# Kernel optimization log

Measured on AMD Instinct MI355X. Metric: run time of the kernel, lower is better.

## Reference

```python
import jax, jax.numpy as jnp
import numpy as np

COEF_MEMORY = 0.2


def setup_inputs() -> dict:
    key = jax.random.key(0)
    k0, k1, k2, k3 = jax.random.split(key, 4)
    bs, T, h, w, ck, cv, M = 8, 8, 32, 32, 256, 3, 512
    return {
        "k": jax.random.normal(k0, (bs, T, h, w, ck), dtype=jnp.float32),
        "v": jax.random.normal(k1, (bs, T, h, w, cv), dtype=jnp.float32),
        "m_k": jax.random.normal(k2, (bs, T, M, ck), dtype=jnp.float32),
        "m_v": jax.random.normal(k3, (bs, T, M, cv), dtype=jnp.float32),
    }


def reference(k, v, m_k, m_v):
    # k: [bs, T, h, w, ck]; v: [bs, T, h, w, cv]
    # m_k: [bs, T, M, ck]; m_v: [bs, T, M, cv]
    bs, T, h, w, ck = k.shape
    cv = v.shape[-1]
    hw = h * w
    k_flat = k.reshape(bs, T, hw, ck)
    v_flat = v.reshape(bs, T, hw, cv)

    # queries: frame i+1 tokens; keys: frame i tokens (unscaled inner product)
    q = k_flat[:, 1:]            # [bs, T-1, hw, ck]
    ref = k_flat[:, :-1]         # [bs, T-1, hw, ck]
    sim_k = jax.nn.softmax(jnp.einsum('btqc,btkc->btqk', q, ref), axis=-1)  # [bs,T-1,hw,hw]
    recon_k = jnp.einsum('btqk,btkv->btqv', sim_k, v_flat[:, :-1])          # [bs,T-1,hw,cv]

    # frame-to-memory attention against memory at step i
    sim_m = jax.nn.softmax(jnp.einsum('btqc,btmc->btqm', q, m_k[:, :-1]), axis=-1)  # [bs,T-1,hw,M]
    recon_m = jnp.einsum('btqm,btmv->btqv', sim_m, m_v[:, :-1])                     # [bs,T-1,hw,cv]

    output_v = (1.0 - COEF_MEMORY) * recon_k + COEF_MEMORY * recon_m  # [bs,T-1,hw,cv]
    ground_truth = v[:, 1:]                                           # [bs,T-1,h,w,cv]
    return output_v, ground_truth
```

## Files before the change

### kernel.cpp

```cpp
#include <hip/hip_runtime.h>
#include <stdint.h>

typedef _Float16 f16x8 __attribute__((ext_vector_type(8)));
typedef __bf16 bf16x8 __attribute__((ext_vector_type(8)));
typedef float f32x4 __attribute__((ext_vector_type(4)));

#define MFMA_F16(a,b,c) __builtin_amdgcn_mfma_f32_16x16x32_f16(a,b,c,0,0,0)
#define MFMA_BF16(a,b,c) __builtin_amdgcn_mfma_f32_16x16x32_bf16(a,b,c,0,0,0)
#define ALPHA 1.2011224087864498f

__device__ __forceinline__ uint32_t f2u(float x){ union{float f;uint32_t u;} c; c.f=x; return c.u; }
__device__ __forceinline__ float u2f(uint32_t u){ union{float f;uint32_t u;} c; c.u=u; return c.f; }

union HU8 { uint32_t u[4]; _Float16 h[8]; f16x8 v; };

__device__ __forceinline__ void split_pair(float x0, float x1, uint32_t& hp, uint32_t& lp){
  uint32_t u0=f2u(x0), u1=f2u(x1);
  uint32_t h0=u0&0xFFFF0000u, h1=u1&0xFFFF0000u;
  hp = (u0>>16) | h1;
  float l0 = x0 - u2f(h0), l1 = x1 - u2f(h1);
  lp = (f2u(l0)>>16) | (f2u(l1)&0xFFFF0000u);
}

__device__ __forceinline__ void glds16(const void* g, void* l){
  __builtin_amdgcn_global_load_lds(
      (const __attribute__((address_space(1))) uint32_t*)(uintptr_t)g,
      (__attribute__((address_space(3))) uint32_t*)(uint32_t)(uintptr_t)l,
      16, 0, 0);
}

__global__ void kast_cvt3(const float* __restrict__ K_, const float* __restrict__ MK_,
                          uint4* __restrict__ khi, uint4* __restrict__ mkhi){
  int i = blockIdx.x*256 + threadIdx.x;
  const float* src; uint4* hi; int j;
  if (i < 2097152){ src = K_;  hi = khi;  j = i; }
  else            { src = MK_; hi = mkhi; j = i - 2097152; }
  const float4* in4 = (const float4*)src;
  float4 a = in4[(size_t)j*2], c = in4[(size_t)j*2+1];
  HU8 h;
  h.h[0]=(_Float16)(a.x*ALPHA); h.h[1]=(_Float16)(a.y*ALPHA);
  h.h[2]=(_Float16)(a.z*ALPHA); h.h[3]=(_Float16)(a.w*ALPHA);
  h.h[4]=(_Float16)(c.x*ALPHA); h.h[5]=(_Float16)(c.y*ALPHA);
  h.h[6]=(_Float16)(c.z*ALPHA); h.h[7]=(_Float16)(c.w*ALPHA);
  hi[j] = make_uint4(h.u[0],h.u[1],h.u[2],h.u[3]);
}

__launch_bounds__(256, 2)
__global__ void kast_attn9(const ushort* __restrict__ khi, const ushort* __restrict__ mkhi,
                           const float* __restrict__ V_, const float* __restrict__ MV_,
                           float* __restrict__ part) {
  __shared__ uint8_t KB[2][16384];
  __shared__ float vlds[1536];

  const int bid = blockIdx.x;
  const int xcd = bid & 7;
  const int idx = bid >> 3;
  const int grp = idx / 24;
  const int sub = idx - grp*24;
  const int s   = xcd + 8*grp;
  const int qb  = sub & 7;
  const int ks  = sub >> 3;
  const int b = s / 7, t = s % 7;

  const uint8_t* kh8; const float* vbase;
  if (ks < 2){
    size_t row0 = (size_t)((b*8 + t)*1024 + ks*512);
    kh8 = (const uint8_t*)khi + row0*512;
    vbase = V_ + row0*3;
  } else {
    size_t row0 = (size_t)((b*8 + t)*512);
    kh8 = (const uint8_t*)mkhi + row0*512;
    vbase = MV_ + row0*3;
  }

  const int tid = threadIdx.x;
  const int w = tid >> 6, l = tid & 63;
  const int lj = l & 15, lq = l >> 4;
  const int qrow0 = qb*128 + w*32;

  for (int i = tid; i < 1536; i += 256) vlds[i] = vbase[i];

  const uint8_t* q8 = (const uint8_t*)khi + (size_t)((b*8 + t + 1)*1024)*512;
  f16x8 qh[2][8];
#pragma unroll
  for (int rt=0; rt<2; rt++){
    const uint8_t* qr = q8 + (size_t)(qrow0 + rt*16 + lj)*512 + lq*16;
#pragma unroll
    for (int kc=0; kc<8; kc++)
      qh[rt][kc] = *(const f16x8*)(qr + kc*64);
  }

  float m[2][4], ssum[2][4], o[2][4][3];
#pragma unroll
  for (int rt=0;rt<2;rt++)
#pragma unroll
    for (int r=0;r<4;r++){
      m[rt][r]=-1e30f; ssum[rt][r]=0.f;
      o[rt][r][0]=0.f; o[rt][r][1]=0.f; o[rt][r][2]=0.f;
    }

  const int sg = l & 31;
  const int rsub = l >> 5;

  #define ISSUE_TILE(NT, P) do{                                              \
    _Pragma("unroll")                                                        \
    for (int i_=0;i_<4;i_++){                                                \
      int lrow_ = (w<<3) + (i_<<1) + rsub;                                   \
      size_t soff_ = (size_t)((NT)*32 + lrow_)*512 + (size_t)((sg ^ (lrow_&7))<<4); \
      uint32_t dbase_ = ((w<<3) + (i_<<1))*512;                              \
      glds16(kh8 + soff_, &KB[(P)][dbase_]);                                 \
    } }while(0)

  ISSUE_TILE(0, 0);
  __syncthreads();

  for (int nt=0; nt<16; nt++){
    const int cur = nt & 1;
    if (nt < 15){
      ISSUE_TILE(nt+1, cur^1);
      asm volatile("s_waitcnt vmcnt(4)" ::: "memory");
    } else {
      asm volatile("s_waitcnt vmcnt(0)" ::: "memory");
    }
    asm volatile("s_barrier" ::: "memory");

    f32x4 acc[2][2];
#pragma unroll
    for (int rt=0;rt<2;rt++){ acc[rt][0]=(f32x4){0,0,0,0}; acc[rt][1]=(f32x4){0,0,0,0}; }

    const int sx = (l&7)<<4;
#pragma unroll
    for (int ct=0;ct<2;ct++){
      const uint8_t* rb = &KB[cur][(ct*16 + lj)*512];
#pragma unroll
      for (int kc=0;kc<8;kc++){
        int bo = (kc*64 + (lq<<4)) ^ sx;
        f16x8 bh = *(const f16x8*)(rb + bo);
        acc[0][ct] = MFMA_F16(qh[0][kc], bh, acc[0][ct]);
        acc[1][ct] = MFMA_F16(qh[1][kc], bh, acc[1][ct]);
      }
    }

    float vv[2][3];
#pragma unroll
    for (int ct=0;ct<2;ct++){
      int c = (nt*32 + ct*16 + lj)*3;
      vv[ct][0]=vlds[c]; vv[ct][1]=vlds[c+1]; vv[ct][2]=vlds[c+2];
    }
#pragma unroll
    for (int rt=0;rt<2;rt++)
#pragma unroll
      for (int r=0;r<4;r++){
        float s0=acc[rt][0][r], s1=acc[rt][1][r];
        float mo = m[rt][r];
        float mn = fmaxf(mo, fmaxf(s0,s1));
        float sc = exp2f(mo - mn);
        float p0 = exp2f(s0 - mn), p1 = exp2f(s1 - mn);
        ssum[rt][r] = ssum[rt][r]*sc + (p0 + p1);
        o[rt][r][0] = o[rt][r][0]*sc + p0*vv[0][0] + p1*vv[1][0];
        o[rt][r][1] = o[rt][r][1]*sc + p0*vv[0][1] + p1*vv[1][1];
        o[rt][r][2] = o[rt][r][2]*sc + p0*vv[0][2] + p1*vv[1][2];
        m[rt][r]=mn;
      }

    asm volatile("s_barrier" ::: "memory");
  }

#pragma unroll
  for (int rt=0;rt<2;rt++)
#pragma unroll
    for (int r=0;r<4;r++){
      float mm = m[rt][r];
      mm = fmaxf(mm, __shfl_xor(mm,1));
      mm = fmaxf(mm, __shfl_xor(mm,2));
      mm = fmaxf(mm, __shfl_xor(mm,4));
      mm = fmaxf(mm, __shfl_xor(mm,8));
      float f = exp2f(m[rt][r]-mm);
      float sl = ssum[rt][r]*f;
      float o0=o[rt][r][0]*f, o1=o[rt][r][1]*f, o2=o[rt][r][2]*f;
      sl += __shfl_xor(sl,1); sl += __shfl_xor(sl,2); sl += __shfl_xor(sl,4); sl += __shfl_xor(sl,8);
      o0 += __shfl_xor(o0,1); o0 += __shfl_xor(o0,2); o0 += __shfl_xor(o0,4); o0 += __shfl_xor(o0,8);
      o1 += __shfl_xor(o1,1); o1 += __shfl_xor(o1,2); o1 += __shfl_xor(o1,4); o1 += __shfl_xor(o1,8);
      o2 += __shfl_xor(o2,1); o2 += __shfl_xor(o2,2); o2 += __shfl_xor(o2,4); o2 += __shfl_xor(o2,8);
      if (lj == 0){
        int prow = qrow0 + rt*16 + lq*4 + r;
        float* pp = part + ((size_t)(s*3 + ks)*1024 + prow)*5;
        pp[0]=mm; pp[1]=sl; pp[2]=o0; pp[3]=o1; pp[4]=o2;
      }
    }
  #undef ISSUE_TILE
}

__global__ void kast_merge(const float* __restrict__ part, float* __restrict__ OUT_){
  int r = blockIdx.x*256 + threadIdx.x;
  if (r >= 56*1024) return;
  int s = r >> 10, row = r & 1023;
  const float* pa = part + ((size_t)(s*3+0)*1024 + row)*5;
  const float* pb = part + ((size_t)(s*3+1)*1024 + row)*5;
  const float* pm = part + ((size_t)(s*3+2)*1024 + row)*5;
  float ma=pa[0], sa=pa[1], mb=pb[0], sb=pb[1];
  float M = fmaxf(ma,mb);
  float ea = exp2f(ma-M), eb = exp2f(mb-M);
  float w1 = 0.8f / (sa*ea + sb*eb);
  float w2 = 0.2f / pm[1];
  float* op = OUT_ + (size_t)(s*1024 + row)*3;
  op[0] = (pa[2]*ea + pb[2]*eb)*w1 + pm[2]*w2;
  op[1] = (pa[3]*ea + pb[3]*eb)*w1 + pm[3]*w2;
  op[2] = (pa[4]*ea + pb[4]*eb)*w1 + pm[4]*w2;
}

__launch_bounds__(256, 2)
__global__ void kast_attn_fb(const float* __restrict__ K_, const float* __restrict__ V_,
                             const float* __restrict__ MK_, const float* __restrict__ MV_,
                             float* __restrict__ OUT_) {
  __shared__ char KhB[64*512];
  __shared__ char KlB[64*512];
  __shared__ float vlds[192];

  const int bid = blockIdx.x;
  const int s  = ((bid>>6)<<3) | (bid & 7);
  const int qb = (bid>>3) & 7;
  const int b = s / 7, t = s % 7;
  const float* qptr = K_ + (size_t)((b*8 + t + 1) * 1024) * 256;
  const float* k1   = K_ + (size_t)((b*8 + t) * 1024) * 256;
  const float* v1   = V_ + (size_t)((b*8 + t) * 1024) * 3;
  const float* k2   = MK_ + (size_t)((b*8 + t) * 512) * 256;
  const float* v2   = MV_ + (size_t)((b*8 + t) * 512) * 3;
  float* outp = OUT_ + (size_t)((b*7 + t) * 1024) * 3;

  const int tid = threadIdx.x;
  const int w = tid >> 6, l = tid & 63;
  const int lj = l & 15, lq = l >> 4;
  const int qrow0 = qb*128 + w*32;

  bf16x8 qh[2][8], ql[2][8];
#pragma unroll
  for (int rt=0; rt<2; rt++){
    const float* qr = qptr + (size_t)(qrow0 + rt*16 + lj)*256 + lq*8;
#pragma unroll
    for (int kc=0; kc<8; kc++){
      float4 a = *(const float4*)(qr + kc*32);
      float4 c = *(const float4*)(qr + kc*32 + 4);
      union { uint32_t d[4]; bf16x8 v; } hh, ll;
      split_pair(a.x, a.y, hh.d[0], ll.d[0]);
      split_pair(a.z, a.w, hh.d[1], ll.d[1]);
      split_pair(c.x, c.y, hh.d[2], ll.d[2]);
      split_pair(c.z, c.w, hh.d[3], ll.d[3]);
      qh[rt][kc]=hh.v; ql[rt][kc]=ll.v;
    }
  }

  for (int ph=0; ph<2; ph++){
    const float* ks = ph ? k2 : k1;
    const float* vs = ph ? v2 : v1;
    const int ntiles = ph ? 8 : 16;
    float m[2][4], ssum[2][4], o[2][4][3];
#pragma unroll
    for (int rt=0;rt<2;rt++)
#pragma unroll
      for (int r=0;r<4;r++){
        m[rt][r]=-1e30f; ssum[rt][r]=0.f;
        o[rt][r][0]=0.f; o[rt][r][1]=0.f; o[rt][r][2]=0.f;
      }

    for (int nt=0; nt<ntiles; nt++){
      __syncthreads();
      const float* kt = ks + (size_t)nt*64*256;
#pragma unroll 4
      for (int i=0;i<16;i++){
        int f4i = tid + i*256;
        int row = f4i >> 6;
        int col4 = f4i & 63;
        float4 x = *(const float4*)(kt + row*256 + col4*4);
        uint32_t hp0,lp0,hp1,lp1;
        split_pair(x.x,x.y,hp0,lp0);
        split_pair(x.z,x.w,hp1,lp1);
        int boff = row*512 + ((col4*8) ^ ((row&7)<<4));
        *(uint2*)(KhB + boff) = make_uint2(hp0,hp1);
        *(uint2*)(KlB + boff) = make_uint2(lp0,lp1);
      }
      if (tid < 192) vlds[tid] = vs[nt*192 + tid];
      __syncthreads();

      f32x4 acc[2][4];
#pragma unroll
      for (int rt=0;rt<2;rt++)
#pragma unroll
        for (int ct=0;ct<4;ct++)
          acc[rt][ct] = (f32x4){0.f,0.f,0.f,0.f};

      const int sx = (l&7)<<4;
#pragma unroll
      for (int ct=0;ct<4;ct++){
        const char* rbh = KhB + (ct*16 + lj)*512;
        const char* rbl = KlB + (ct*16 + lj)*512;
#pragma unroll
        for (int kc=0;kc<8;kc++){
          int bo = (kc*64 + (lq<<4)) ^ sx;
          bf16x8 bh = *(const bf16x8*)(rbh + bo);
          bf16x8 bl = *(const bf16x8*)(rbl + bo);
          acc[0][ct] = MFMA_BF16(qh[0][kc], bh, acc[0][ct]);
          acc[1][ct] = MFMA_BF16(qh[1][kc], bh, acc[1][ct]);
          acc[0][ct] = MFMA_BF16(qh[0][kc], bl, acc[0][ct]);
          acc[1][ct] = MFMA_BF16(qh[1][kc], bl, acc[1][ct]);
          acc[0][ct] = MFMA_BF16(ql[0][kc], bh, acc[0][ct]);
          acc[1][ct] = MFMA_BF16(ql[1][kc], bh, acc[1][ct]);
        }
      }

      float vv[4][3];
#pragma unroll
      for (int ct=0;ct<4;ct++){
        int c = (ct*16 + lj)*3;
        vv[ct][0]=vlds[c]; vv[ct][1]=vlds[c+1]; vv[ct][2]=vlds[c+2];
      }
#pragma unroll
      for (int rt=0;rt<2;rt++)
#pragma unroll
        for (int r=0;r<4;r++){
          float s0=acc[rt][0][r], s1=acc[rt][1][r], s2=acc[rt][2][r], s3=acc[rt][3][r];
          float tmax = fmaxf(fmaxf(s0,s1),fmaxf(s2,s3));
          float mo = m[rt][r];
          float mn = fmaxf(mo, tmax);
          float sc = __expf(mo - mn);
          float p0=__expf(s0-mn), p1=__expf(s1-mn), p2=__expf(s2-mn), p3=__expf(s3-mn);
          ssum[rt][r] = ssum[rt][r]*sc + ((p0+p1)+(p2+p3));
          o[rt][r][0] = o[rt][r][0]*sc + (p0*vv[0][0]+p1*vv[1][0]) + (p2*vv[2][0]+p3*vv[3][0]);
          o[rt][r][1] = o[rt][r][1]*sc + (p0*vv[0][1]+p1*vv[1][1]) + (p2*vv[2][1]+p3*vv[3][1]);
          o[rt][r][2] = o[rt][r][2]*sc + (p0*vv[0][2]+p1*vv[1][2]) + (p2*vv[2][2]+p3*vv[3][2]);
          m[rt][r]=mn;
        }
    }

    const float coef = ph ? 0.2f : 0.8f;
#pragma unroll
    for (int rt=0;rt<2;rt++)
#pragma unroll
      for (int r=0;r<4;r++){
        float mm = m[rt][r];
        mm = fmaxf(mm, __shfl_xor(mm,1));
        mm = fmaxf(mm, __shfl_xor(mm,2));
        mm = fmaxf(mm, __shfl_xor(mm,4));
        mm = fmaxf(mm, __shfl_xor(mm,8));
        float f = __expf(m[rt][r]-mm);
        float sl = ssum[rt][r]*f;
        float o0=o[rt][r][0]*f, o1=o[rt][r][1]*f, o2=o[rt][r][2]*f;
        sl += __shfl_xor(sl,1); sl += __shfl_xor(sl,2); sl += __shfl_xor(sl,4); sl += __shfl_xor(sl,8);
        o0 += __shfl_xor(o0,1); o0 += __shfl_xor(o0,2); o0 += __shfl_xor(o0,4); o0 += __shfl_xor(o0,8);
        o1 += __shfl_xor(o1,1); o1 += __shfl_xor(o1,2); o1 += __shfl_xor(o1,4); o1 += __shfl_xor(o1,8);
        o2 += __shfl_xor(o2,1); o2 += __shfl_xor(o2,2); o2 += __shfl_xor(o2,4); o2 += __shfl_xor(o2,8);
        if (lj == 0){
          int row = qrow0 + rt*16 + lq*4 + r;
          float* op = outp + (size_t)row*3;
          float invs = coef / sl;
          if (ph==0){ op[0]=o0*invs; op[1]=o1*invs; op[2]=o2*invs; }
          else      { op[0]+=o0*invs; op[1]+=o1*invs; op[2]+=o2*invs; }
        }
      }
  }
}

__global__ void kast_gt(const float* __restrict__ V_, float* __restrict__ OUT_){
  int s = blockIdx.x; int b = s/7, t = s%7;
  const float4* src = (const float4*)(V_ + (size_t)(b*8+t+1)*3072);
  float4* dst = (float4*)(OUT_ + 172032 + (size_t)s*3072);
  for (int i=threadIdx.x; i<768; i+=256) dst[i] = src[i];
}

extern "C" void kernel_launch(void* const* d_in, const int* in_sizes, int n_in,
                              void* d_out, int out_size, void* d_ws, size_t ws_size,
                              hipStream_t stream) {
  (void)in_sizes; (void)n_in; (void)out_size;
  const float* K_  = (const float*)d_in[0];
  const float* V_  = (const float*)d_in[1];
  const float* MK_ = (const float*)d_in[2];
  const float* MV_ = (const float*)d_in[3];
  float* out = (float*)d_out;

  const size_t NEED = 53772288;
  if (ws_size >= NEED){
    uint8_t* w8 = (uint8_t*)d_ws;
    ushort* khi  = (ushort*)(w8);
    ushort* mkhi = (ushort*)(w8 + 33554432);
    float*  part = (float*)(w8 + 50331648);
    hipLaunchKernelGGL(kast_cvt3, dim3(12288), dim3(256), 0, stream, K_, MK_,
                       (uint4*)khi, (uint4*)mkhi);
    hipLaunchKernelGGL(kast_attn9, dim3(1344), dim3(256), 0, stream, khi, mkhi, V_, MV_, part);
    hipLaunchKernelGGL(kast_merge, dim3(224),  dim3(256), 0, stream, part, out);
  } else {
    hipLaunchKernelGGL(kast_attn_fb, dim3(448), dim3(256), 0, stream, K_, V_, MK_, MV_, out);
  }
  hipLaunchKernelGGL(kast_gt, dim3(56), dim3(256), 0, stream, V_, out);
}
```

Measured before the change: 124.7 us.

## Load key tiles directly into registers and skip softmax rescale lazily

Drops the LDS double-buffered global_load_lds staging of key tiles and the per-iteration barriers. Each wave now loads its B operands straight from global memory into registers, software-pipelined between two 16-column halves, and raises wave priority around MFMA bursts. It also adds a lazy online-softmax rescale that only updates the running max when a new score exceeds it by more than 24 (log2 units). The cost is that all four waves redundantly fetch the same key rows from global/L2 instead of sharing them through LDS, and the register load rises.

```diff
diff --git a/kernel.cpp b/kernel.cpp
--- a/kernel.cpp
+++ b/kernel.cpp
@@ -20,13 +20,6 @@
   hp = (u0>>16) | h1;
   float l0 = x0 - u2f(h0), l1 = x1 - u2f(h1);
   lp = (f2u(l0)>>16) | (f2u(l1)&0xFFFF0000u);
-}
-
-__device__ __forceinline__ void glds16(const void* g, void* l){
-  __builtin_amdgcn_global_load_lds(
-      (const __attribute__((address_space(1))) uint32_t*)(uintptr_t)g,
-      (__attribute__((address_space(3))) uint32_t*)(uint32_t)(uintptr_t)l,
-      16, 0, 0);
 }
 
 __global__ void kast_cvt3(const float* __restrict__ K_, const float* __restrict__ MK_,
@@ -46,10 +39,9 @@
 }
 
 __launch_bounds__(256, 2)
-__global__ void kast_attn9(const ushort* __restrict__ khi, const ushort* __restrict__ mkhi,
-                           const float* __restrict__ V_, const float* __restrict__ MV_,
-                           float* __restrict__ part) {
-  __shared__ uint8_t KB[2][16384];
+__global__ void kast_attn10(const ushort* __restrict__ khi, const ushort* __restrict__ mkhi,
+                            const float* __restrict__ V_, const float* __restrict__ MV_,
+                            float* __restrict__ part) {
   __shared__ float vlds[1536];
 
   const int bid = blockIdx.x;
@@ -89,6 +81,7 @@
     for (int kc=0; kc<8; kc++)
       qh[rt][kc] = *(const f16x8*)(qr + kc*64);
   }
+  __syncthreads();
 
   float m[2][4], ssum[2][4], o[2][4][3];
 #pragma unroll
@@ -99,47 +92,42 @@
       o[rt][r][0]=0.f; o[rt][r][1]=0.f; o[rt][r][2]=0.f;
     }
 
-  const int sg = l & 31;
-  const int rsub = l >> 5;
-
-  #define ISSUE_TILE(NT, P) do{                                              \
-    _Pragma("unroll")                                                        \
-    for (int i_=0;i_<4;i_++){                                                \
-      int lrow_ = (w<<3) + (i_<<1) + rsub;                                   \
-      size_t soff_ = (size_t)((NT)*32 + lrow_)*512 + (size_t)((sg ^ (lrow_&7))<<4); \
-      uint32_t dbase_ = ((w<<3) + (i_<<1))*512;                              \
-      glds16(kh8 + soff_, &KB[(P)][dbase_]);                                 \
-    } }while(0)
-
-  ISSUE_TILE(0, 0);
-  __syncthreads();
+  const uint8_t* kp0 = kh8 + (size_t)(lj*512 + lq*16);
+  const uint8_t* kp1 = kp0 + 16*512;
+
+  f16x8 ka[8], kb[8];
+#pragma unroll
+  for (int kc=0;kc<8;kc++) ka[kc] = *(const f16x8*)(kp0 + kc*64);
 
   for (int nt=0; nt<16; nt++){
-    const int cur = nt & 1;
+#pragma unroll
+    for (int kc=0;kc<8;kc++) kb[kc] = *(const f16x8*)(kp1 + kc*64);
+
+    f32x4 acc[2][2];
+#pragma unroll
+    for (int rt=0;rt<2;rt++){ acc[rt][0]=(f32x4){0,0,0,0}; acc[rt][1]=(f32x4){0,0,0,0}; }
+
+    __builtin_amdgcn_s_setprio(1);
+#pragma unroll
+    for (int kc=0;kc<8;kc++){
+      acc[0][0] = MFMA_F16(qh[0][kc], ka[kc], acc[0][0]);
+      acc[1][0] = MFMA_F16(qh[1][kc], ka[kc], acc[1][0]);
+    }
+    __builtin_amdgcn_s_setprio(0);
+
+    kp0 += 16384; kp1 += 16384;
     if (nt < 15){
-      ISSUE_TILE(nt+1, cur^1);
-      asm volatile("s_waitcnt vmcnt(4)" ::: "memory");
-    } else {
-      asm volatile("s_waitcnt vmcnt(0)" ::: "memory");
-    }
-    asm volatile("s_barrier" ::: "memory");
-
-    f32x4 acc[2][2];
-#pragma unroll
-    for (int rt=0;rt<2;rt++){ acc[rt][0]=(f32x4){0,0,0,0}; acc[rt][1]=(f32x4){0,0,0,0}; }
-
-    const int sx = (l&7)<<4;
-#pragma unroll
-    for (int ct=0;ct<2;ct++){
-      const uint8_t* rb = &KB[cur][(ct*16 + lj)*512];
-#pragma unroll
-      for (int kc=0;kc<8;kc++){
-        int bo = (kc*64 + (lq<<4)) ^ sx;
-        f16x8 bh = *(const f16x8*)(rb + bo);
-        acc[0][ct] = MFMA_F16(qh[0][kc], bh, acc[0][ct]);
-        acc[1][ct] = MFMA_F16(qh[1][kc], bh, acc[1][ct]);
-      }
-    }
+#pragma unroll
+      for (int kc=0;kc<8;kc++) ka[kc] = *(const f16x8*)(kp0 + kc*64);
+    }
+
+    __builtin_amdgcn_s_setprio(1);
+#pragma unroll
+    for (int kc=0;kc<8;kc++){
+      acc[0][1] = MFMA_F16(qh[0][kc], kb[kc], acc[0][1]);
+      acc[1][1] = MFMA_F16(qh[1][kc], kb[kc], acc[1][1]);
+    }
+    __builtin_amdgcn_s_setprio(0);
 
     float vv[2][3];
 #pragma unroll
@@ -147,23 +135,38 @@
       int c = (nt*32 + ct*16 + lj)*3;
       vv[ct][0]=vlds[c]; vv[ct][1]=vlds[c+1]; vv[ct][2]=vlds[c+2];
     }
+    float pm[2][4];
+    float need = -1e30f;
 #pragma unroll
     for (int rt=0;rt<2;rt++)
 #pragma unroll
       for (int r=0;r<4;r++){
-        float s0=acc[rt][0][r], s1=acc[rt][1][r];
-        float mo = m[rt][r];
-        float mn = fmaxf(mo, fmaxf(s0,s1));
-        float sc = exp2f(mo - mn);
-        float p0 = exp2f(s0 - mn), p1 = exp2f(s1 - mn);
-        ssum[rt][r] = ssum[rt][r]*sc + (p0 + p1);
-        o[rt][r][0] = o[rt][r][0]*sc + p0*vv[0][0] + p1*vv[1][0];
-        o[rt][r][1] = o[rt][r][1]*sc + p0*vv[0][1] + p1*vv[1][1];
-        o[rt][r][2] = o[rt][r][2]*sc + p0*vv[0][2] + p1*vv[1][2];
-        m[rt][r]=mn;
-      }
-
-    asm volatile("s_barrier" ::: "memory");
+        pm[rt][r] = fmaxf(acc[rt][0][r], acc[rt][1][r]);
+        need = fmaxf(need, pm[rt][r] - m[rt][r]);
+      }
+    if (need > 24.f){
+#pragma unroll
+      for (int rt=0;rt<2;rt++)
+#pragma unroll
+        for (int r=0;r<4;r++){
+          float mn = fmaxf(m[rt][r], pm[rt][r]);
+          float sc = exp2f(m[rt][r] - mn);
+          ssum[rt][r] *= sc;
+          o[rt][r][0] *= sc; o[rt][r][1] *= sc; o[rt][r][2] *= sc;
+          m[rt][r] = mn;
+        }
+    }
+#pragma unroll
+    for (int rt=0;rt<2;rt++)
+#pragma unroll
+      for (int r=0;r<4;r++){
+        float p0 = exp2f(acc[rt][0][r] - m[rt][r]);
+        float p1 = exp2f(acc[rt][1][r] - m[rt][r]);
+        ssum[rt][r] += p0 + p1;
+        o[rt][r][0] += p0*vv[0][0] + p1*vv[1][0];
+        o[rt][r][1] += p0*vv[0][1] + p1*vv[1][1];
+        o[rt][r][2] += p0*vv[0][2] + p1*vv[1][2];
+      }
   }
 
 #pragma unroll
@@ -188,7 +191,6 @@
         pp[0]=mm; pp[1]=sl; pp[2]=o0; pp[3]=o1; pp[4]=o2;
       }
     }
-  #undef ISSUE_TILE
 }
 
 __global__ void kast_merge(const float* __restrict__ part, float* __restrict__ OUT_){
@@ -385,7 +387,7 @@
     float*  part = (float*)(w8 + 50331648);
     hipLaunchKernelGGL(kast_cvt3, dim3(12288), dim3(256), 0, stream, K_, MK_,
                        (uint4*)khi, (uint4*)mkhi);
-    hipLaunchKernelGGL(kast_attn9, dim3(1344), dim3(256), 0, stream, khi, mkhi, V_, MV_, part);
+    hipLaunchKernelGGL(kast_attn10, dim3(1344), dim3(256), 0, stream, khi, mkhi, V_, MV_, part);
     hipLaunchKernelGGL(kast_merge, dim3(224),  dim3(256), 0, stream, part, out);
   } else {
     hipLaunchKernelGGL(kast_attn_fb, dim3(448), dim3(256), 0, stream, K_, V_, MK_, MV_, out);
```

Measured after the change: 214.9 us. +72.4%, slower.

## Double block size to 512 threads and add lazy softmax rescaling

Applied to the files above, without the earlier changes.

Each attention block now uses 8 waves covering 256 query rows instead of 4 waves covering 128, so each K tile staged in LDS is reused by twice as many queries and each thread issues half as many async loads. The online softmax now skips the running-max rescale unless some row's new max exceeds the stored max by more than a threshold of 24 in log2 units. This saves exp2 calls and multiplies per tile. The trade-offs are half as many blocks, one block per CU under the new launch bounds, and wider barriers across 8 waves. The rescale threshold relies on fp32 headroom to avoid overflow.

```diff
diff --git a/kernel.cpp b/kernel.cpp
--- a/kernel.cpp
+++ b/kernel.cpp
@@ -45,21 +45,21 @@
   hi[j] = make_uint4(h.u[0],h.u[1],h.u[2],h.u[3]);
 }
 
-__launch_bounds__(256, 2)
-__global__ void kast_attn9(const ushort* __restrict__ khi, const ushort* __restrict__ mkhi,
-                           const float* __restrict__ V_, const float* __restrict__ MV_,
-                           float* __restrict__ part) {
+__launch_bounds__(512, 1)
+__global__ void kast_attn11(const ushort* __restrict__ khi, const ushort* __restrict__ mkhi,
+                            const float* __restrict__ V_, const float* __restrict__ MV_,
+                            float* __restrict__ part) {
   __shared__ uint8_t KB[2][16384];
   __shared__ float vlds[1536];
 
   const int bid = blockIdx.x;
   const int xcd = bid & 7;
   const int idx = bid >> 3;
-  const int grp = idx / 24;
-  const int sub = idx - grp*24;
+  const int grp = idx / 12;
+  const int sub = idx - grp*12;
   const int s   = xcd + 8*grp;
-  const int qb  = sub & 7;
-  const int ks  = sub >> 3;
+  const int qbB = sub & 3;
+  const int ks  = sub >> 2;
   const int b = s / 7, t = s % 7;
 
   const uint8_t* kh8; const float* vbase;
@@ -76,9 +76,9 @@
   const int tid = threadIdx.x;
   const int w = tid >> 6, l = tid & 63;
   const int lj = l & 15, lq = l >> 4;
-  const int qrow0 = qb*128 + w*32;
-
-  for (int i = tid; i < 1536; i += 256) vlds[i] = vbase[i];
+  const int qrow0 = qbB*256 + w*32;
+
+  for (int i = tid; i < 1536; i += 512) vlds[i] = vbase[i];
 
   const uint8_t* q8 = (const uint8_t*)khi + (size_t)((b*8 + t + 1)*1024)*512;
   f16x8 qh[2][8];
@@ -104,10 +104,10 @@
 
   #define ISSUE_TILE(NT, P) do{                                              \
     _Pragma("unroll")                                                        \
-    for (int i_=0;i_<4;i_++){                                                \
-      int lrow_ = (w<<3) + (i_<<1) + rsub;                                   \
+    for (int i_=0;i_<2;i_++){                                                \
+      int lrow_ = (w<<2) + (i_<<1) + rsub;                                   \
       size_t soff_ = (size_t)((NT)*32 + lrow_)*512 + (size_t)((sg ^ (lrow_&7))<<4); \
-      uint32_t dbase_ = ((w<<3) + (i_<<1))*512;                              \
+      uint32_t dbase_ = ((w<<2) + (i_<<1))*512;                              \
       glds16(kh8 + soff_, &KB[(P)][dbase_]);                                 \
     } }while(0)
 
@@ -118,7 +118,7 @@
     const int cur = nt & 1;
     if (nt < 15){
       ISSUE_TILE(nt+1, cur^1);
-      asm volatile("s_waitcnt vmcnt(4)" ::: "memory");
+      asm volatile("s_waitcnt vmcnt(2)" ::: "memory");
     } else {
       asm volatile("s_waitcnt vmcnt(0)" ::: "memory");
     }
@@ -147,20 +147,37 @@
       int c = (nt*32 + ct*16 + lj)*3;
       vv[ct][0]=vlds[c]; vv[ct][1]=vlds[c+1]; vv[ct][2]=vlds[c+2];
     }
+    float pm[2][4];
+    float need = -1e30f;
 #pragma unroll
     for (int rt=0;rt<2;rt++)
 #pragma unroll
       for (int r=0;r<4;r++){
-        float s0=acc[rt][0][r], s1=acc[rt][1][r];
-        float mo = m[rt][r];
-        float mn = fmaxf(mo, fmaxf(s0,s1));
-        float sc = exp2f(mo - mn);
-        float p0 = exp2f(s0 - mn), p1 = exp2f(s1 - mn);
-        ssum[rt][r] = ssum[rt][r]*sc + (p0 + p1);
-        o[rt][r][0] = o[rt][r][0]*sc + p0*vv[0][0] + p1*vv[1][0];
-        o[rt][r][1] = o[rt][r][1]*sc + p0*vv[0][1] + p1*vv[1][1];
-        o[rt][r][2] = o[rt][r][2]*sc + p0*vv[0][2] + p1*vv[1][2];
-        m[rt][r]=mn;
+        pm[rt][r] = fmaxf(acc[rt][0][r], acc[rt][1][r]);
+        need = fmaxf(need, pm[rt][r] - m[rt][r]);
+      }
+    if (need > 24.f){
+#pragma unroll
+      for (int rt=0;rt<2;rt++)
+#pragma unroll
+        for (int r=0;r<4;r++){
+          float mn = fmaxf(m[rt][r], pm[rt][r]);
+          float sc = exp2f(m[rt][r] - mn);
+          ssum[rt][r] *= sc;
+          o[rt][r][0] *= sc; o[rt][r][1] *= sc; o[rt][r][2] *= sc;
+          m[rt][r] = mn;
+        }
+    }
+#pragma unroll
+    for (int rt=0;rt<2;rt++)
+#pragma unroll
+      for (int r=0;r<4;r++){
+        float p0 = exp2f(acc[rt][0][r] - m[rt][r]);
+        float p1 = exp2f(acc[rt][1][r] - m[rt][r]);
+        ssum[rt][r] += p0 + p1;
+        o[rt][r][0] += p0*vv[0][0] + p1*vv[1][0];
+        o[rt][r][1] += p0*vv[0][1] + p1*vv[1][1];
+        o[rt][r][2] += p0*vv[0][2] + p1*vv[1][2];
       }
 
     asm volatile("s_barrier" ::: "memory");
@@ -385,7 +402,7 @@
     float*  part = (float*)(w8 + 50331648);
     hipLaunchKernelGGL(kast_cvt3, dim3(12288), dim3(256), 0, stream, K_, MK_,
                        (uint4*)khi, (uint4*)mkhi);
-    hipLaunchKernelGGL(kast_attn9, dim3(1344), dim3(256), 0, stream, khi, mkhi, V_, MV_, part);
+    hipLaunchKernelGGL(kast_attn11, dim3(672), dim3(512), 0, stream, khi, mkhi, V_, MV_, part);
     hipLaunchKernelGGL(kast_merge, dim3(224),  dim3(256), 0, stream, part, out);
   } else {
     hipLaunchKernelGGL(kast_attn_fb, dim3(448), dim3(256), 0, stream, K_, V_, MK_, MV_, out);
```

Measured after the change: 141.4 us. 1.13x slower.
